# Performance work log

Hardware: AMD Instinct MI355X
Metric: run time of the kernel (lower is better)

## Reference

```python
import jax, jax.numpy as jnp
import numpy as np

N_U, N_M = 60000, 20000
F_U, F_M = 64, 128
IN_C, HID, OUT_C = 256, 256, 128
N = N_U + N_M
E = 500000
BN_EPS = 1e-5


def gcn_conv(z, W, b, src, dst, n):
    # PyG GCNConv: h = z @ W; add self-loops; symmetric norm D^-1/2 (A+I) D^-1/2; scatter-add; + bias
    h = z @ W                                        # [n, out]
    loop = jnp.arange(n)
    src_sl = jnp.concatenate([src, loop])            # [E+n]
    dst_sl = jnp.concatenate([dst, loop])
    deg = jax.ops.segment_sum(jnp.ones_like(dst_sl, h.dtype), dst_sl, num_segments=n)
    dinv = jax.lax.rsqrt(deg)                        # deg >= 1 due to self-loops
    norm = dinv[src_sl] * dinv[dst_sl]               # [E+n]
    msg = h[src_sl] * norm[:, None]                  # gather + scale
    out = jax.ops.segment_sum(msg, dst_sl, num_segments=n)
    return out + b


def batch_norm(z, gamma, beta):
    mean = jnp.mean(z, axis=0)
    var = jnp.var(z, axis=0)                         # biased, as torch BN uses for normalization
    return (z - mean) * jax.lax.rsqrt(var + BN_EPS) * gamma + beta


def setup_inputs() -> dict:
    key = jax.random.key(0)
    ks = jax.random.split(key, 13)
    x = jax.random.normal(ks[0], (N_U, F_U), jnp.float32)
    y = jax.random.normal(ks[1], (N_M, F_M), jnp.float32)
    edge_index = jax.random.randint(ks[2], (2, E), 0, N, dtype=jnp.int64)
    def lin(k, fin, fout):
        s = 1.0 / np.sqrt(fin)
        kw, kb = jax.random.split(k)
        return (jax.random.uniform(kw, (fin, fout), jnp.float32, -s, s),
                jax.random.uniform(kb, (fout,), jnp.float32, -s, s))
    fc1_w, fc1_b = lin(ks[3], F_U, IN_C)
    fc2_w, fc2_b = lin(ks[4], F_M, IN_C)
    conv1_w, conv1_b = lin(ks[5], IN_C, HID)
    conv2_w, conv2_b = lin(ks[6], HID, OUT_C)
    bn_gamma = jnp.ones((HID,), jnp.float32)
    bn_beta = jnp.zeros((HID,), jnp.float32)
    return {"x": x, "y": y, "edge_index": edge_index,
            "fc1_w": fc1_w, "fc1_b": fc1_b, "fc2_w": fc2_w, "fc2_b": fc2_b,
            "conv1_w": conv1_w, "conv1_b": conv1_b, "conv2_w": conv2_w, "conv2_b": conv2_b,
            "bn_gamma": bn_gamma, "bn_beta": bn_beta}


def reference(x, y, edge_index, fc1_w, fc1_b, fc2_w, fc2_b,
              conv1_w, conv1_b, conv2_w, conv2_b, bn_gamma, bn_beta):
    src, dst = edge_index[0], edge_index[1]
    xu = x @ fc1_w + fc1_b                           # [N_U, IN_C]
    xm = y @ fc2_w + fc2_b                           # [N_M, IN_C]
    z = jnp.concatenate([xu, xm], axis=0)            # [N, IN_C]
    z = gcn_conv(z, conv1_w, conv1_b, src, dst, N)   # [N, HID]
    z = jax.nn.relu(batch_norm(z, bn_gamma, bn_beta))
    z = gcn_conv(z, conv2_w, conv2_b, src, dst, N)   # [N, OUT_C]
    return z
```

## Files before the change

### kernel.cpp

```cpp
#include <hip/hip_runtime.h>
#include <math.h>
#include <stdint.h>

#define N_U 60000
#define N_M 20000
#define NN  80000
#define EE  500000
#define BN_EPS 1e-5f
#define NB_SCAN 313

typedef __attribute__((ext_vector_type(8))) short short8v;
typedef __attribute__((ext_vector_type(4))) float f32x4;

__device__ __forceinline__ unsigned short bf_hi(float f) {
    unsigned u = __float_as_uint(f);
    return (unsigned short)((u + 0x7FFFu + ((u >> 16) & 1u)) >> 16);
}
__device__ __forceinline__ float bf_f(unsigned short h) {
    return __uint_as_float(((unsigned)h) << 16);
}

__global__ void prep_kernel(const int* __restrict__ ei32, int* __restrict__ cnt,
                            int* __restrict__ cursor, int* __restrict__ rowptr,
                            float* __restrict__ sums, float* __restrict__ sumsq,
                            int* __restrict__ flag) {
    int i = blockIdx.x * blockDim.x + threadIdx.x;
    if (i < 256) { sums[i] = 0.f; sumsq[i] = 0.f; }
    for (int j = i; j < NN; j += gridDim.x * blockDim.x) { cnt[j] = 0; cursor[j] = 0; }
    if (i == 0) rowptr[NN] = EE;
    if (blockIdx.x == 0) {
        __shared__ int nz;
        if (threadIdx.x == 0) nz = 0;
        __syncthreads();
        int v = ei32[2 * threadIdx.x + 1];
        if (v != 0) atomicOr(&nz, 1);
        __syncthreads();
        if (threadIdx.x == 0) *flag = (nz == 0) ? 1 : 0;
    }
}

__device__ __forceinline__ int load_idx(const void* ei, int f, int pos) {
    return f ? (int)((const long long*)ei)[pos] : ((const int*)ei)[pos];
}

__global__ void hist_kernel(const void* __restrict__ ei, const int* __restrict__ flag,
                            int* __restrict__ cnt) {
    int f = *flag;
    int stride = gridDim.x * blockDim.x;
    for (int e = blockIdx.x * blockDim.x + threadIdx.x; e < EE; e += stride) {
        int d = load_idx(ei, f, EE + e);
        atomicAdd(&cnt[d], 1);
    }
}

__global__ void dinv_kernel(const int* __restrict__ cnt, float* __restrict__ dinv) {
    int i = blockIdx.x * blockDim.x + threadIdx.x;
    if (i < NN) dinv[i] = rsqrtf(1.0f + (float)cnt[i]);
}

__global__ void scan1_kernel(const int* __restrict__ cnt, int* __restrict__ rowptr,
                             int* __restrict__ blockSums) {
    __shared__ int sh[256];
    int tid = threadIdx.x;
    int i = blockIdx.x * 256 + tid;
    int v = (i < NN) ? cnt[i] : 0;
    int x = v;
    sh[tid] = x; __syncthreads();
#pragma unroll
    for (int off = 1; off < 256; off <<= 1) {
        int t = (tid >= off) ? sh[tid - off] : 0;
        __syncthreads();
        x += t; sh[tid] = x;
        __syncthreads();
    }
    if (i < NN) rowptr[i] = x - v;
    if (tid == 255) blockSums[blockIdx.x] = x;
}

__global__ void scan2_kernel(int* __restrict__ blockSums) {
    __shared__ int sh[512];
    int tid = threadIdx.x;
    int v = (tid < NB_SCAN) ? blockSums[tid] : 0;
    int x = v;
    sh[tid] = x; __syncthreads();
#pragma unroll
    for (int off = 1; off < 512; off <<= 1) {
        int t = (tid >= off) ? sh[tid - off] : 0;
        __syncthreads();
        x += t; sh[tid] = x;
        __syncthreads();
    }
    if (tid < NB_SCAN) blockSums[tid] = x - v;
}

__global__ void scan3_kernel(int* __restrict__ rowptr, const int* __restrict__ blockSums) {
    int i = blockIdx.x * 256 + threadIdx.x;
    if (i < NN) rowptr[i] += blockSums[blockIdx.x];
}

__global__ void fill_kernel(const void* __restrict__ ei, const int* __restrict__ flag,
                            const int* __restrict__ rowptr, int* __restrict__ cursor,
                            int* __restrict__ csr_src) {
    int f = *flag;
    int stride = gridDim.x * blockDim.x;
    for (int e = blockIdx.x * blockDim.x + threadIdx.x; e < EE; e += stride) {
        int s = load_idx(ei, f, e);
        int d = load_idx(ei, f, EE + e);
        int pos = rowptr[d] + atomicAdd(&cursor[d], 1);
        csr_src[pos] = s;
    }
}

template <int K, int N>
__global__ void wsplit_frag_kernel(const float* __restrict__ W,
                                   short* __restrict__ Hi, short* __restrict__ Lo) {
    int i = blockIdx.x * 256 + threadIdx.x;
    if (i >= K * N) return;
    int k = i / N, n = i - k * N;
    float v = W[i];
    unsigned short h = bf_hi(v);
    unsigned short l = bf_hi(v - bf_f(h));
    int nt = n >> 4, r = n & 15, kt = k >> 5, q = (k >> 3) & 3, p = k & 7;
    int idx = ((nt * (K / 32) + kt) << 9) + (q << 7) + (r << 3) + p;
    Hi[idx] = (short)h;
    Lo[idx] = (short)l;
}

template <int K, int N, int MODE, bool BNRELU, bool OUTBF16>
__global__ __launch_bounds__(256) void mfma_gemm_kernel(
    int M, const float* __restrict__ A, const short* __restrict__ WfHi,
    const short* __restrict__ WfLo, const float* __restrict__ ep,
    const float* __restrict__ bnsc, const float* __restrict__ bnsh,
    float* __restrict__ Out, short* __restrict__ OutB) {
    constexpr int LDT = 40;
    constexpr int NT = K / 32;
    __shared__ short AsHi[128 * LDT];
    __shared__ short AsLo[128 * LDT];
    const int tid  = threadIdx.x;
    const int lane = tid & 63, wave = tid >> 6;
    const int wm = (wave >> 1) * 64, wn = (wave & 1) * 64;
    const int R0 = blockIdx.x * 128;
    const int n0 = blockIdx.y * 128;
    const int srow  = tid >> 1;
    const int shalf = (tid & 1) * 16;
    const int l15  = lane & 15;
    const int koff = (lane >> 4) * 8;
    const int nt0  = (n0 + wn) >> 4;

    f32x4 acc[4][4];
#pragma unroll
    for (int mi = 0; mi < 4; ++mi)
#pragma unroll
        for (int ni = 0; ni < 4; ++ni)
            acc[mi][ni] = (f32x4){0.f, 0.f, 0.f, 0.f};

    const int arow = min(R0 + srow, M - 1);
    const float* abase = &A[(size_t)arow * K + shalf];

    float4 a0 = ((const float4*)abase)[0];
    float4 a1 = ((const float4*)abase)[1];
    float4 a2 = ((const float4*)abase)[2];
    float4 a3 = ((const float4*)abase)[3];

#pragma unroll
    for (int kt = 0; kt < NT; ++kt) {
        const int k0 = kt * 32;

        if (BNRELU) {
            const float4* gs = (const float4*)&bnsc[k0 + shalf];
            const float4* gh = (const float4*)&bnsh[k0 + shalf];
            float4 s0 = gs[0], s1 = gs[1], s2 = gs[2], s3 = gs[3];
            float4 t0 = gh[0], t1 = gh[1], t2 = gh[2], t3 = gh[3];
#define BNR4(a, s, t)                                                          \
            a.x = fmaxf(a.x * s.x + t.x, 0.f);                                 \
            a.y = fmaxf(a.y * s.y + t.y, 0.f);                                 \
            a.z = fmaxf(a.z * s.z + t.z, 0.f);                                 \
            a.w = fmaxf(a.w * s.w + t.w, 0.f);
            BNR4(a0, s0, t0); BNR4(a1, s1, t1); BNR4(a2, s2, t2); BNR4(a3, s3, t3);
#undef BNR4
        }

        unsigned h[8], l[8];
#define SPLIT4(v, hA, hB, lA, lB)                                              \
        {                                                                      \
            unsigned short h0_ = bf_hi(v.x), h1_ = bf_hi(v.y);                 \
            unsigned short h2_ = bf_hi(v.z), h3_ = bf_hi(v.w);                 \
            unsigned short l0_ = bf_hi(v.x - bf_f(h0_));                       \
            unsigned short l1_ = bf_hi(v.y - bf_f(h1_));                       \
            unsigned short l2_ = bf_hi(v.z - bf_f(h2_));                       \
            unsigned short l3_ = bf_hi(v.w - bf_f(h3_));                       \
            hA = (unsigned)h0_ | ((unsigned)h1_ << 16);                        \
            hB = (unsigned)h2_ | ((unsigned)h3_ << 16);                        \
            lA = (unsigned)l0_ | ((unsigned)l1_ << 16);                        \
            lB = (unsigned)l2_ | ((unsigned)l3_ << 16);                        \
        }
        SPLIT4(a0, h[0], h[1], l[0], l[1]);
        SPLIT4(a1, h[2], h[3], l[2], l[3]);
        SPLIT4(a2, h[4], h[5], l[4], l[5]);
        SPLIT4(a3, h[6], h[7], l[6], l[7]);
#undef SPLIT4

        __syncthreads();
        int4* dAH = (int4*)&AsHi[srow * LDT + shalf];
        int4* dAL = (int4*)&AsLo[srow * LDT + shalf];
        dAH[0] = make_int4((int)h[0], (int)h[1], (int)h[2], (int)h[3]);
        dAH[1] = make_int4((int)h[4], (int)h[5], (int)h[6], (int)h[7]);
        dAL[0] = make_int4((int)l[0], (int)l[1], (int)l[2], (int)l[3]);
        dAL[1] = make_int4((int)l[4], (int)l[5], (int)l[6], (int)l[7]);
        __syncthreads();

        if (kt + 1 < NT) {
            const float4* gnext = (const float4*)(abase + (kt + 1) * 32);
            a0 = gnext[0]; a1 = gnext[1]; a2 = gnext[2]; a3 = gnext[3];
        }

        short8v bh[4], bl[4];
#pragma unroll
        for (int ni = 0; ni < 4; ++ni) {
            int fidx = (((nt0 + ni) * NT + kt) << 9) + lane * 8;
            bh[ni] = *(const short8v*)&WfHi[fidx];
            bl[ni] = *(const short8v*)&WfLo[fidx];
        }

#pragma unroll
        for (int mi = 0; mi < 4; ++mi) {
            int mrow = wm + mi * 16 + l15;
            short8v ah = *(const short8v*)&AsHi[mrow * LDT + koff];
            short8v al = *(const short8v*)&AsLo[mrow * LDT + koff];
#pragma unroll
            for (int ni = 0; ni < 4; ++ni) {
                acc[mi][ni] = __builtin_amdgcn_mfma_f32_16x16x32_bf16(ah, bh[ni], acc[mi][ni], 0, 0, 0);
                acc[mi][ni] = __builtin_amdgcn_mfma_f32_16x16x32_bf16(ah, bl[ni], acc[mi][ni], 0, 0, 0);
                acc[mi][ni] = __builtin_amdgcn_mfma_f32_16x16x32_bf16(al, bh[ni], acc[mi][ni], 0, 0, 0);
            }
        }
    }

#pragma unroll
    for (int mi = 0; mi < 4; ++mi) {
#pragma unroll
        for (int i = 0; i < 4; ++i) {
            int row = R0 + wm + mi * 16 + (lane >> 4) * 4 + i;
            if (row < M) {
                float sc = (MODE == 0) ? ep[row] : 1.0f;
#pragma unroll
                for (int ni = 0; ni < 4; ++ni) {
                    int col = n0 + wn + ni * 16 + l15;
                    float v = acc[mi][ni][i];
                    v = (MODE == 0) ? v * sc : v + ep[col];
                    if (OUTBF16)
                        OutB[(size_t)row * N + col] = (short)bf_hi(v);
                    else
                        Out[(size_t)row * N + col] = v;
                }
            }
        }
    }
}

__device__ __forceinline__ void acc_bf4(float4& a, ushort4 v) {
    a.x += bf_f(v.x); a.y += bf_f(v.y); a.z += bf_f(v.z); a.w += bf_f(v.w);
}

__global__ __launch_bounds__(256) void gather256_kernel(const short* __restrict__ h,
                                                        const float* __restrict__ bias,
                                                        const float* __restrict__ dinv,
                                                        const int* __restrict__ rowptr,
                                                        const int* __restrict__ csr_src,
                                                        float* __restrict__ out) {
    int wid = threadIdx.x >> 6, lane = threadIdx.x & 63;
    int r = blockIdx.x * 4 + wid;
    if (r >= NN) return;
    int beg = rowptr[r], end = rowptr[r + 1];
    float dr = dinv[r];
    const ushort4* hp = (const ushort4*)h;
    float4 acc = {0.f, 0.f, 0.f, 0.f};
    acc_bf4(acc, hp[(size_t)r * 64 + lane]);
    int k = beg;
    for (; k + 3 < end; k += 4) {
        int s0 = csr_src[k], s1 = csr_src[k + 1], s2 = csr_src[k + 2], s3 = csr_src[k + 3];
        ushort4 v0 = hp[(size_t)s0 * 64 + lane];
        ushort4 v1 = hp[(size_t)s1 * 64 + lane];
        ushort4 v2 = hp[(size_t)s2 * 64 + lane];
        ushort4 v3 = hp[(size_t)s3 * 64 + lane];
        acc_bf4(acc, v0); acc_bf4(acc, v1); acc_bf4(acc, v2); acc_bf4(acc, v3);
    }
    for (; k < end; ++k)
        acc_bf4(acc, hp[(size_t)csr_src[k] * 64 + lane]);
    float4 b = ((const float4*)bias)[lane];
    float4 o;
    o.x = b.x + dr * acc.x; o.y = b.y + dr * acc.y;
    o.z = b.z + dr * acc.z; o.w = b.w + dr * acc.w;
    ((float4*)(out + (size_t)r * 256))[lane] = o;
}

__global__ __launch_bounds__(256) void gather128_kernel(const short* __restrict__ h,
                                                        const float* __restrict__ bias,
                                                        const float* __restrict__ dinv,
                                                        const int* __restrict__ rowptr,
                                                        const int* __restrict__ csr_src,
                                                        float* __restrict__ out) {
    int sub = threadIdx.x >> 5, lane = threadIdx.x & 31;
    int r = blockIdx.x * 8 + sub;
    if (r >= NN) return;
    int beg = rowptr[r], end = rowptr[r + 1];
    float dr = dinv[r];
    const ushort4* hp = (const ushort4*)h;
    float4 acc = {0.f, 0.f, 0.f, 0.f};
    acc_bf4(acc, hp[(size_t)r * 32 + lane]);
    int k = beg;
    for (; k + 3 < end; k += 4) {
        int s0 = csr_src[k], s1 = csr_src[k + 1], s2 = csr_src[k + 2], s3 = csr_src[k + 3];
        ushort4 v0 = hp[(size_t)s0 * 32 + lane];
        ushort4 v1 = hp[(size_t)s1 * 32 + lane];
        ushort4 v2 = hp[(size_t)s2 * 32 + lane];
        ushort4 v3 = hp[(size_t)s3 * 32 + lane];
        acc_bf4(acc, v0); acc_bf4(acc, v1); acc_bf4(acc, v2); acc_bf4(acc, v3);
    }
    for (; k < end; ++k)
        acc_bf4(acc, hp[(size_t)csr_src[k] * 32 + lane]);
    float4 b = ((const float4*)bias)[lane];
    float4 o;
    o.x = b.x + dr * acc.x; o.y = b.y + dr * acc.y;
    o.z = b.z + dr * acc.z; o.w = b.w + dr * acc.w;
    ((float4*)(out + (size_t)r * 128))[lane] = o;
}

__global__ __launch_bounds__(256) void bn_stats_kernel(const float* __restrict__ a,
                                                       float* __restrict__ sums,
                                                       float* __restrict__ sumsq) {
    __shared__ float shs[256], shs2[256];
    int tid = threadIdx.x;
    int wid = tid >> 6, lane = tid & 63;
    shs[tid] = 0.f; shs2[tid] = 0.f;
    __syncthreads();
    float4 s = {0.f, 0.f, 0.f, 0.f}, s2 = {0.f, 0.f, 0.f, 0.f};
    for (int row = blockIdx.x * 4 + wid; row < NN; row += gridDim.x * 4) {
        float4 v = ((const float4*)(a + (size_t)row * 256))[lane];
        s.x += v.x; s.y += v.y; s.z += v.z; s.w += v.w;
        s2.x += v.x * v.x; s2.y += v.y * v.y; s2.z += v.z * v.z; s2.w += v.w * v.w;
    }
    atomicAdd(&shs[4 * lane + 0], s.x);  atomicAdd(&shs2[4 * lane + 0], s2.x);
    atomicAdd(&shs[4 * lane + 1], s.y);  atomicAdd(&shs2[4 * lane + 1], s2.y);
    atomicAdd(&shs[4 * lane + 2], s.z);  atomicAdd(&shs2[4 * lane + 2], s2.z);
    atomicAdd(&shs[4 * lane + 3], s.w);  atomicAdd(&shs2[4 * lane + 3], s2.w);
    __syncthreads();
    atomicAdd(&sums[tid], shs[tid]);
    atomicAdd(&sumsq[tid], shs2[tid]);
}

__global__ void bn_final_kernel(const float* __restrict__ sums, const float* __restrict__ sumsq,
                                const float* __restrict__ gamma, const float* __restrict__ beta,
                                float* __restrict__ scale, float* __restrict__ shift) {
    int c = threadIdx.x;
    const float Nf = (float)NN;
    float mean = sums[c] / Nf;
    float var = sumsq[c] / Nf - mean * mean;
    float sc = gamma[c] * rsqrtf(var + BN_EPS);
    scale[c] = sc;
    shift[c] = beta[c] - mean * sc;
}

extern "C" void kernel_launch(void* const* d_in, const int* in_sizes, int n_in,
                              void* d_out, int out_size, void* d_ws, size_t ws_size,
                              hipStream_t stream) {
    const float* x       = (const float*)d_in[0];
    const float* y       = (const float*)d_in[1];
    const void*  ei      = d_in[2];
    const float* fc1_w   = (const float*)d_in[3];
    const float* fc1_b   = (const float*)d_in[4];
    const float* fc2_w   = (const float*)d_in[5];
    const float* fc2_b   = (const float*)d_in[6];
    const float* conv1_w = (const float*)d_in[7];
    const float* conv1_b = (const float*)d_in[8];
    const float* conv2_w = (const float*)d_in[9];
    const float* conv2_b = (const float*)d_in[10];
    const float* gamma   = (const float*)d_in[11];
    const float* beta    = (const float*)d_in[12];
    float* out = (float*)d_out;

    float* ws = (float*)d_ws;
    float* bufA = ws;
    float* bufB = ws + (size_t)NN * 256;
    float* aux  = bufB + (size_t)NN * 256;
    float* dinv  = aux;
    float* sums  = dinv + NN;
    float* sumsq = sums + 256;
    float* scale = sumsq + 256;
    float* shift = scale + 256;
    int*   flag      = (int*)(shift + 256);
    int*   cnt       = flag + 1;
    int*   rowptr    = cnt + NN;
    int*   cursor    = rowptr + NN + 1;
    int*   blockSums = cursor + NN;
    int*   csr_src   = blockSums + NB_SCAN + 3;
    short* w1th = (short*)(((uintptr_t)(csr_src + EE) + 15) & ~(uintptr_t)15);
    short* w1tl = w1th + 256 * 256;
    short* w2th = w1tl + 256 * 256;
    short* w2tl = w2th + 256 * 128;
    short* wf1h = w2tl + 256 * 128;
    short* wf1l = wf1h + 256 * 64;
    short* wf2h = wf1l + 256 * 64;
    short* wf2l = wf2h + 256 * 128;
    short* hB   = (short*)bufB;

    prep_kernel<<<320, 256, 0, stream>>>((const int*)ei, cnt, cursor, rowptr, sums, sumsq, flag);
    hist_kernel<<<1024, 256, 0, stream>>>(ei, flag, cnt);
    dinv_kernel<<<(NN + 255) / 256, 256, 0, stream>>>(cnt, dinv);
    scan1_kernel<<<NB_SCAN, 256, 0, stream>>>(cnt, rowptr, blockSums);
    scan2_kernel<<<1, 512, 0, stream>>>(blockSums);
    scan3_kernel<<<NB_SCAN, 256, 0, stream>>>(rowptr, blockSums);
    fill_kernel<<<1024, 256, 0, stream>>>(ei, flag, rowptr, cursor, csr_src);
    wsplit_frag_kernel<256, 256><<<256, 256, 0, stream>>>(conv1_w, w1th, w1tl);
    wsplit_frag_kernel<256, 128><<<128, 256, 0, stream>>>(conv2_w, w2th, w2tl);
    wsplit_frag_kernel<64, 256><<<64, 256, 0, stream>>>(fc1_w, wf1h, wf1l);
    wsplit_frag_kernel<128, 256><<<128, 256, 0, stream>>>(fc2_w, wf2h, wf2l);

    mfma_gemm_kernel<64, 256, 1, false, false><<<dim3(469, 2), 256, 0, stream>>>(
        N_U, x, wf1h, wf1l, fc1_b, nullptr, nullptr, bufA, nullptr);
    mfma_gemm_kernel<128, 256, 1, false, false><<<dim3(157, 2), 256, 0, stream>>>(
        N_M, y, wf2h, wf2l, fc2_b, nullptr, nullptr, bufA + (size_t)N_U * 256, nullptr);

    mfma_gemm_kernel<256, 256, 0, false, true><<<dim3(625, 2), 256, 0, stream>>>(
        NN, bufA, w1th, w1tl, dinv, nullptr, nullptr, nullptr, hB);
    gather256_kernel<<<NN / 4, 256, 0, stream>>>(hB, conv1_b, dinv, rowptr, csr_src, bufA);

    bn_stats_kernel<<<256, 256, 0, stream>>>(bufA, sums, sumsq);
    bn_final_kernel<<<1, 256, 0, stream>>>(sums, sumsq, gamma, beta, scale, shift);

    mfma_gemm_kernel<256, 128, 0, true, true><<<dim3(625, 1), 256, 0, stream>>>(
        NN, bufA, w2th, w2tl, dinv, scale, shift, nullptr, hB);
    gather128_kernel<<<NN / 8, 256, 0, stream>>>(hB, conv2_b, dinv, rowptr, csr_src, out);
}
```

Measured before the change: 398.8 us.

## Emit pre-split bf16 hi/lo from input GEMMs and merge small setup kernels

```diff
diff --git a/kernel.cpp b/kernel.cpp
--- a/kernel.cpp
+++ b/kernel.cpp
@@ -53,13 +53,8 @@
     }
 }
 
-__global__ void dinv_kernel(const int* __restrict__ cnt, float* __restrict__ dinv) {
-    int i = blockIdx.x * blockDim.x + threadIdx.x;
-    if (i < NN) dinv[i] = rsqrtf(1.0f + (float)cnt[i]);
-}
-
 __global__ void scan1_kernel(const int* __restrict__ cnt, int* __restrict__ rowptr,
-                             int* __restrict__ blockSums) {
+                             int* __restrict__ blockSums, float* __restrict__ dinv) {
     __shared__ int sh[256];
     int tid = threadIdx.x;
     int i = blockIdx.x * 256 + tid;
@@ -73,7 +68,10 @@
         x += t; sh[tid] = x;
         __syncthreads();
     }
-    if (i < NN) rowptr[i] = x - v;
+    if (i < NN) {
+        rowptr[i] = x - v;
+        dinv[i] = rsqrtf(1.0f + (float)v);
+    }
     if (tid == 255) blockSums[blockIdx.x] = x;
 }
 
@@ -111,11 +109,8 @@
     }
 }
 
-template <int K, int N>
-__global__ void wsplit_frag_kernel(const float* __restrict__ W,
-                                   short* __restrict__ Hi, short* __restrict__ Lo) {
-    int i = blockIdx.x * 256 + threadIdx.x;
-    if (i >= K * N) return;
+__device__ __forceinline__ void wfrag_store(const float* W, short* Hi, short* Lo,
+                                            int i, int K, int N) {
     int k = i / N, n = i - k * N;
     float v = W[i];
     unsigned short h = bf_hi(v);
@@ -126,12 +121,27 @@
     Lo[idx] = (short)l;
 }
 
-template <int K, int N, int MODE, bool BNRELU, bool OUTBF16>
+__global__ void wsplit_all_kernel(const float* __restrict__ W1, const float* __restrict__ W2,
+                                  const float* __restrict__ Wf1, const float* __restrict__ Wf2,
+                                  short* __restrict__ W1h, short* __restrict__ W1l,
+                                  short* __restrict__ W2h, short* __restrict__ W2l,
+                                  short* __restrict__ F1h, short* __restrict__ F1l,
+                                  short* __restrict__ F2h, short* __restrict__ F2l) {
+    int i = blockIdx.x * 256 + threadIdx.x;
+    if (i < 256 * 256) wfrag_store(W1, W1h, W1l, i, 256, 256);
+    if (i < 256 * 128) wfrag_store(W2, W2h, W2l, i, 256, 128);
+    if (i < 64 * 256)  wfrag_store(Wf1, F1h, F1l, i, 64, 256);
+    if (i < 128 * 256) wfrag_store(Wf2, F2h, F2l, i, 128, 256);
+}
+
+template <int K, int N, int MODE, int AIN, bool BNRELU, int OUTK>
 __global__ __launch_bounds__(256) void mfma_gemm_kernel(
-    int M, const float* __restrict__ A, const short* __restrict__ WfHi,
-    const short* __restrict__ WfLo, const float* __restrict__ ep,
-    const float* __restrict__ bnsc, const float* __restrict__ bnsh,
-    float* __restrict__ Out, short* __restrict__ OutB) {
+    int M, const float* __restrict__ A,
+    const short* __restrict__ AHi, const short* __restrict__ ALo,
+    const short* __restrict__ WfHi, const short* __restrict__ WfLo,
+    const float* __restrict__ ep, const float* __restrict__ bnsc,
+    const float* __restrict__ bnsh,
+    float* __restrict__ Out, short* __restrict__ OutB, short* __restrict__ OutL) {
     constexpr int LDT = 40;
     constexpr int NT = K / 32;
     __shared__ short AsHi[128 * LDT];
@@ -155,63 +165,82 @@
             acc[mi][ni] = (f32x4){0.f, 0.f, 0.f, 0.f};
 
     const int arow = min(R0 + srow, M - 1);
-    const float* abase = &A[(size_t)arow * K + shalf];
-
-    float4 a0 = ((const float4*)abase)[0];
-    float4 a1 = ((const float4*)abase)[1];
-    float4 a2 = ((const float4*)abase)[2];
-    float4 a3 = ((const float4*)abase)[3];
+    const float* abase = (AIN == 0) ? &A[(size_t)arow * K + shalf] : nullptr;
+    const short* ahb   = (AIN == 1) ? &AHi[(size_t)arow * K + shalf] : nullptr;
+    const short* alb   = (AIN == 1) ? &ALo[(size_t)arow * K + shalf] : nullptr;
+
+    float4 a0, a1, a2, a3;
+    int4 th0, th1, tl0, tl1;
+    if constexpr (AIN == 0) {
+        const float4* ga = (const float4*)abase;
+        a0 = ga[0]; a1 = ga[1]; a2 = ga[2]; a3 = ga[3];
+    } else {
+        th0 = ((const int4*)ahb)[0]; th1 = ((const int4*)ahb)[1];
+        tl0 = ((const int4*)alb)[0]; tl1 = ((const int4*)alb)[1];
+    }
 
 #pragma unroll
     for (int kt = 0; kt < NT; ++kt) {
         const int k0 = kt * 32;
-
-        if (BNRELU) {
-            const float4* gs = (const float4*)&bnsc[k0 + shalf];
-            const float4* gh = (const float4*)&bnsh[k0 + shalf];
-            float4 s0 = gs[0], s1 = gs[1], s2 = gs[2], s3 = gs[3];
-            float4 t0 = gh[0], t1 = gh[1], t2 = gh[2], t3 = gh[3];
+        int4 sh0, sh1, sl0, sl1;
+
+        if constexpr (AIN == 0) {
+            if (BNRELU) {
+                const float4* gs = (const float4*)&bnsc[k0 + shalf];
+                const float4* gh = (const float4*)&bnsh[k0 + shalf];
+                float4 s0 = gs[0], s1 = gs[1], s2 = gs[2], s3 = gs[3];
+                float4 t0 = gh[0], t1 = gh[1], t2 = gh[2], t3 = gh[3];
 #define BNR4(a, s, t)                                                          \
-            a.x = fmaxf(a.x * s.x + t.x, 0.f);                                 \
-            a.y = fmaxf(a.y * s.y + t.y, 0.f);                                 \
-            a.z = fmaxf(a.z * s.z + t.z, 0.f);                                 \
-            a.w = fmaxf(a.w * s.w + t.w, 0.f);
-            BNR4(a0, s0, t0); BNR4(a1, s1, t1); BNR4(a2, s2, t2); BNR4(a3, s3, t3);
+                a.x = fmaxf(a.x * s.x + t.x, 0.f);                             \
+                a.y = fmaxf(a.y * s.y + t.y, 0.f);                             \
+                a.z = fmaxf(a.z * s.z + t.z, 0.f);                             \
+                a.w = fmaxf(a.w * s.w + t.w, 0.f);
+                BNR4(a0, s0, t0); BNR4(a1, s1, t1); BNR4(a2, s2, t2); BNR4(a3, s3, t3);
 #undef BNR4
+            }
+            unsigned h[8], l[8];
+#define SPLIT4(v, hA, hB, lA, lB)                                              \
+            {                                                                  \
+                unsigned short h0_ = bf_hi(v.x), h1_ = bf_hi(v.y);             \
+                unsigned short h2_ = bf_hi(v.z), h3_ = bf_hi(v.w);             \
+                unsigned short l0_ = bf_hi(v.x - bf_f(h0_));                   \
+                unsigned short l1_ = bf_hi(v.y - bf_f(h1_));                   \
+                unsigned short l2_ = bf_hi(v.z - bf_f(h2_));                   \
+                unsigned short l3_ = bf_hi(v.w - bf_f(h3_));                   \
+                hA = (unsigned)h0_ | ((unsigned)h1_ << 16);                    \
+                hB = (unsigned)h2_ | ((unsigned)h3_ << 16);                    \
+                lA = (unsigned)l0_ | ((unsigned)l1_ << 16);                    \
+                lB = (unsigned)l2_ | ((unsigned)l3_ << 16);                    \
+            }
+            SPLIT4(a0, h[0], h[1], l[0], l[1]);
+            SPLIT4(a1, h[2], h[3], l[2], l[3]);
+            SPLIT4(a2, h[4], h[5], l[4], l[5]);
+            SPLIT4(a3, h[6], h[7], l[6], l[7]);
+#undef SPLIT4
+            sh0 = make_int4((int)h[0], (int)h[1], (int)h[2], (int)h[3]);
+            sh1 = make_int4((int)h[4], (int)h[5], (int)h[6], (int)h[7]);
+            sl0 = make_int4((int)l[0], (int)l[1], (int)l[2], (int)l[3]);
+            sl1 = make_int4((int)l[4], (int)l[5], (int)l[6], (int)l[7]);
+        } else {
+            sh0 = th0; sh1 = th1; sl0 = tl0; sl1 = tl1;
         }
-
-        unsigned h[8], l[8];
-#define SPLIT4(v, hA, hB, lA, lB)                                              \
-        {                                                                      \
-            unsigned short h0_ = bf_hi(v.x), h1_ = bf_hi(v.y);                 \
-            unsigned short h2_ = bf_hi(v.z), h3_ = bf_hi(v.w);                 \
-            unsigned short l0_ = bf_hi(v.x - bf_f(h0_));                       \
-            unsigned short l1_ = bf_hi(v.y - bf_f(h1_));                       \
-            unsigned short l2_ = bf_hi(v.z - bf_f(h2_));                       \
-            unsigned short l3_ = bf_hi(v.w - bf_f(h3_));                       \
-            hA = (unsigned)h0_ | ((unsigned)h1_ << 16);                        \
-            hB = (unsigned)h2_ | ((unsigned)h3_ << 16);                        \
-            lA = (unsigned)l0_ | ((unsigned)l1_ << 16);                        \
-            lB = (unsigned)l2_ | ((unsigned)l3_ << 16);                        \
-        }
-        SPLIT4(a0, h[0], h[1], l[0], l[1]);
-        SPLIT4(a1, h[2], h[3], l[2], l[3]);
-        SPLIT4(a2, h[4], h[5], l[4], l[5]);
-        SPLIT4(a3, h[6], h[7], l[6], l[7]);
-#undef SPLIT4
 
         __syncthreads();
         int4* dAH = (int4*)&AsHi[srow * LDT + shalf];
         int4* dAL = (int4*)&AsLo[srow * LDT + shalf];
-        dAH[0] = make_int4((int)h[0], (int)h[1], (int)h[2], (int)h[3]);
-        dAH[1] = make_int4((int)h[4], (int)h[5], (int)h[6], (int)h[7]);
-        dAL[0] = make_int4((int)l[0], (int)l[1], (int)l[2], (int)l[3]);
-        dAL[1] = make_int4((int)l[4], (int)l[5], (int)l[6], (int)l[7]);
+        dAH[0] = sh0; dAH[1] = sh1;
+        dAL[0] = sl0; dAL[1] = sl1;
         __syncthreads();
 
         if (kt + 1 < NT) {
-            const float4* gnext = (const float4*)(abase + (kt + 1) * 32);
-            a0 = gnext[0]; a1 = gnext[1]; a2 = gnext[2]; a3 = gnext[3];
+            if constexpr (AIN == 0) {
+                const float4* gnext = (const float4*)(abase + (kt + 1) * 32);
+                a0 = gnext[0]; a1 = gnext[1]; a2 = gnext[2]; a3 = gnext[3];
+            } else {
+                const int4* gh = (const int4*)(ahb + (kt + 1) * 32);
+                const int4* gl = (const int4*)(alb + (kt + 1) * 32);
+                th0 = gh[0]; th1 = gh[1]; tl0 = gl[0]; tl1 = gl[1];
+            }
         }
 
         short8v bh[4], bl[4];
@@ -248,10 +277,15 @@
                     int col = n0 + wn + ni * 16 + l15;
                     float v = acc[mi][ni][i];
                     v = (MODE == 0) ? v * sc : v + ep[col];
-                    if (OUTBF16)
+                    if constexpr (OUTK == 0) {
+                        Out[(size_t)row * N + col] = v;
+                    } else if constexpr (OUTK == 1) {
                         OutB[(size_t)row * N + col] = (short)bf_hi(v);
-                    else
-                        Out[(size_t)row * N + col] = v;
+                    } else {
+                        unsigned short h = bf_hi(v);
+                        OutB[(size_t)row * N + col] = (short)h;
+                        OutL[(size_t)row * N + col] = (short)bf_hi(v - bf_f(h));
+                    }
                 }
             }
         }
@@ -402,33 +436,39 @@
     short* wf1l = wf1h + 256 * 64;
     short* wf2h = wf1l + 256 * 64;
     short* wf2l = wf2h + 256 * 128;
-    short* hB   = (short*)bufB;
+
+    short* zHi = (short*)bufB;
+    short* zLo = zHi + (size_t)NN * 256;
+    short* hA  = (short*)bufA;
+    float* a1  = bufB;
 
     prep_kernel<<<320, 256, 0, stream>>>((const int*)ei, cnt, cursor, rowptr, sums, sumsq, flag);
     hist_kernel<<<1024, 256, 0, stream>>>(ei, flag, cnt);
-    dinv_kernel<<<(NN + 255) / 256, 256, 0, stream>>>(cnt, dinv);
-    scan1_kernel<<<NB_SCAN, 256, 0, stream>>>(cnt, rowptr, blockSums);
+    scan1_kernel<<<NB_SCAN, 256, 0, stream>>>(cnt, rowptr, blockSums, dinv);
     scan2_kernel<<<1, 512, 0, stream>>>(blockSums);
     scan3_kernel<<<NB_SCAN, 256, 0, stream>>>(rowptr, blockSums);
     fill_kernel<<<1024, 256, 0, stream>>>(ei, flag, rowptr, cursor, csr_src);
-    wsplit_frag_kernel<256, 256><<<256, 256, 0, stream>>>(conv1_w, w1th, w1tl);
-    wsplit_frag_kernel<256, 128><<<128, 256, 0, stream>>>(conv2_w, w2th, w2tl);
-    wsplit_frag_kernel<64, 256><<<64, 256, 0, stream>>>(fc1_w, wf1h, wf1l);
-    wsplit_frag_kernel<128, 256><<<128, 256, 0, stream>>>(fc2_w, wf2h, wf2l);
-
-    mfma_gemm_kernel<64, 256, 1, false, false><<<dim3(469, 2), 256, 0, stream>>>(
-        N_U, x, wf1h, wf1l, fc1_b, nullptr, nullptr, bufA, nullptr);
-    mfma_gemm_kernel<128, 256, 1, false, false><<<dim3(157, 2), 256, 0, stream>>>(
-        N_M, y, wf2h, wf2l, fc2_b, nullptr, nullptr, bufA + (size_t)N_U * 256, nullptr);
-
-    mfma_gemm_kernel<256, 256, 0, false, true><<<dim3(625, 2), 256, 0, stream>>>(
-        NN, bufA, w1th, w1tl, dinv, nullptr, nullptr, nullptr, hB);
-    gather256_kernel<<<NN / 4, 256, 0, stream>>>(hB, conv1_b, dinv, rowptr, csr_src, bufA);
-
-    bn_stats_kernel<<<256, 256, 0, stream>>>(bufA, sums, sumsq);
+    wsplit_all_kernel<<<256, 256, 0, stream>>>(conv1_w, conv2_w, fc1_w, fc2_w,
+                                               w1th, w1tl, w2th, w2tl,
+                                               wf1h, wf1l, wf2h, wf2l);
+
+    mfma_gemm_kernel<64, 256, 1, 0, false, 2><<<dim3(469, 2), 256, 0, stream>>>(
+        N_U, x, nullptr, nullptr, wf1h, wf1l, fc1_b, nullptr, nullptr,
+        nullptr, zHi, zLo);
+    mfma_gemm_kernel<128, 256, 1, 0, false, 2><<<dim3(157, 2), 256, 0, stream>>>(
+        N_M, y, nullptr, nullptr, wf2h, wf2l, fc2_b, nullptr, nullptr,
+        nullptr, zHi + (size_t)N_U * 256, zLo + (size_t)N_U * 256);
+
+    mfma_gemm_kernel<256, 256, 0, 1, false, 1><<<dim3(625, 2), 256, 0, stream>>>(
+        NN, nullptr, zHi, zLo, w1th, w1tl, dinv, nullptr, nullptr,
+        nullptr, hA, nullptr);
+    gather256_kernel<<<NN / 4, 256, 0, stream>>>(hA, conv1_b, dinv, rowptr, csr_src, a1);
+
+    bn_stats_kernel<<<256, 256, 0, stream>>>(a1, sums, sumsq);
     bn_final_kernel<<<1, 256, 0, stream>>>(sums, sumsq, gamma, beta, scale, shift);
 
-    mfma_gemm_kernel<256, 128, 0, true, true><<<dim3(625, 1), 256, 0, stream>>>(
-        NN, bufA, w2th, w2tl, dinv, scale, shift, nullptr, hB);
-    gather128_kernel<<<NN / 8, 256, 0, stream>>>(hB, conv2_b, dinv, rowptr, csr_src, out);
-}
+    mfma_gemm_kernel<256, 128, 0, 0, true, 1><<<dim3(625, 1), 256, 0, stream>>>(
+        NN, a1, nullptr, nullptr, w2th, w2tl, dinv, scale, shift,
+        nullptr, hA, nullptr);
+    gather128_kernel<<<NN / 8, 256, 0, stream>>>(hA, conv2_b, dinv, rowptr, csr_src, out);
+}
```

New measurement: 403.0 us. About the same (+1.0%).
